# Kernel optimization log

Measured on AMD Instinct MI355X. Metric: run time of the kernel, lower is better.

## Reference

```python
import jax, jax.numpy as jnp
import numpy as np

B, Q, H, V = 32, 180, 768, 19004


def setup_inputs() -> dict:
    key = jax.random.key(0)
    k1, k2, k3, k4 = jax.random.split(key, 4)
    output_tokens = jax.random.normal(k1, (B, Q, H), dtype=jnp.float32)
    W_embed = jax.random.normal(k2, (V, H), dtype=jnp.float32) * 0.02
    b_embed = jax.random.normal(k3, (V,), dtype=jnp.float32) * 0.02
    parcel_ids = jax.random.randint(k4, (V,), 0, Q, dtype=jnp.int32)
    return {"output_tokens": output_tokens, "W_embed": W_embed,
            "b_embed": b_embed, "parcel_ids": parcel_ids}


def reference(output_tokens, W_embed, b_embed, parcel_ids):
    # embed: Linear(hidden_dim -> num_hemi_voxels): [B, Q, V]
    pred = jnp.einsum('bqh,vh->bqv', output_tokens, W_embed) + b_embed
    # movedim(1, -1): [B, V, Q]
    pred = jnp.moveaxis(pred, 1, -1)
    # parcel_mask: one-hot [V, Q] (each voxel assigned to exactly one parcel)
    num_q = output_tokens.shape[1]
    mask = jax.nn.one_hot(parcel_ids, num_q, dtype=pred.dtype)  # [V, Q]
    # multiply by mask and sum over parcel/query axis -> [B, V]
    return jnp.sum(pred * mask, axis=-1)
```

## Files before the change

### kernel.cpp

```cpp
#include <hip/hip_runtime.h>
#include <hip/hip_bf16.h>

#define BB 32
#define QQ 180
#define HH 768
#define VV 19004
#define VB 64
#define KH 384
#define SB 19008
#define MAXDESC 480
#define STRIDE 392

#define WS_NTOT   2048
#define WS_SORTED 4096
#define WS_POSOF  81920
#define WS_DESC   159744
#define WS_RES    167936

typedef __attribute__((ext_vector_type(8))) short short8v;
typedef __attribute__((ext_vector_type(4))) float f32x4;

__device__ __forceinline__ short f2bf(float f) {
    unsigned u = __builtin_bit_cast(unsigned, f);
    u += 0x7FFFu + ((u >> 16) & 1u);
    return (short)(u >> 16);
}

__global__ void prep_k(const int* __restrict__ pid, int* __restrict__ sorted,
                       int* __restrict__ posOf, int4* __restrict__ desc,
                       int* __restrict__ ntot) {
    __shared__ int cnt[256];
    __shared__ int sc[256];
    __shared__ int sn[256];
    __shared__ int cur[256];
    const int t = threadIdx.x;
    if (t < 256) cnt[t] = 0;
    __syncthreads();
    for (int v = t; v < VV; v += 1024) atomicAdd(&cnt[pid[v]], 1);
    __syncthreads();
    if (t < 256) sc[t] = cnt[t];
    __syncthreads();
    for (int off = 1; off < 256; off <<= 1) {
        int add = (t < 256 && t >= off) ? sc[t - off] : 0;
        __syncthreads();
        if (t < 256) sc[t] += add;
        __syncthreads();
    }
    if (t < 256) {
        const int c = cnt[t];
        cur[t] = sc[t] - c;
        sn[t] = (c + VB - 1) / VB;
    }
    __syncthreads();
    for (int off = 1; off < 256; off <<= 1) {
        int add = (t < 256 && t >= off) ? sn[t - off] : 0;
        __syncthreads();
        if (t < 256) sn[t] += add;
        __syncthreads();
    }
    if (t < QQ) {
        const int c = cnt[t];
        const int nch = (c + VB - 1) / VB;
        const int cb = sn[t] - nch;
        const int qs = cur[t];
        for (int j = 0; j < nch; ++j)
            desc[cb + j] = make_int4(t, qs + j * VB, min(VB, c - j * VB), 0);
    }
    if (t == 255) *ntot = sn[255];
    __syncthreads();
    for (int v = t; v < VV; v += 1024) {
        const int q = pid[v];
        const int pos = atomicAdd(&cur[q], 1);
        sorted[pos] = v;
        posOf[v] = pos;
    }
}

__launch_bounds__(256)
__global__ void main_k(const float* __restrict__ OT, const float* __restrict__ W,
                       const int* __restrict__ sorted, const int4* __restrict__ desc,
                       const int* __restrict__ ntot, float* __restrict__ res) {
    const int nt = *ntot;
    const int bid = blockIdx.x;
    const int ci = bid >> 1;
    if (ci >= nt) return;
    const int kh = bid & 1;
    const int4 d = desc[ci];
    const int q     = __builtin_amdgcn_readfirstlane(d.x);
    const int start = __builtin_amdgcn_readfirstlane(d.y);
    const int len   = __builtin_amdgcn_readfirstlane(d.z);
    const int tid = threadIdx.x;

    __shared__ short OTlds[BB * STRIDE];

    {
        const int r = tid >> 3;
        const int o = tid & 7;
        const float* src = OT + ((size_t)r * QQ + q) * HH + kh * KH + o * 8;
        short* dst = &OTlds[r * STRIDE + o * 8];
#pragma unroll
        for (int it = 0; it < 6; ++it) {
            const float4 f0 = *(const float4*)(src + it * 64);
            const float4 f1 = *(const float4*)(src + it * 64 + 4);
            short8v s;
            s[0] = f2bf(f0.x); s[1] = f2bf(f0.y); s[2] = f2bf(f0.z); s[3] = f2bf(f0.w);
            s[4] = f2bf(f1.x); s[5] = f2bf(f1.y); s[6] = f2bf(f1.z); s[7] = f2bf(f1.w);
            *(short8v*)(dst + it * 64) = s;
        }
    }

    const int lane = tid & 63;
    const int w = tid >> 6;
    const int co = lane & 15;
    const int kq = lane >> 4;
    const int vl = 16 * w + co;
    const int vg = sorted[start + min(vl, len - 1)];
    const float4* wp4 = (const float4*)(W + (size_t)vg * HH + kh * KH + kq * 8);
    const short* a0 = &OTlds[co * STRIDE + kq * 8];

    float4 wf[24];
#pragma unroll
    for (int kk = 0; kk < 12; ++kk) {
        wf[2 * kk]     = wp4[kk * 8];
        wf[2 * kk + 1] = wp4[kk * 8 + 1];
    }

    __syncthreads();

    f32x4 acc0 = {0.f, 0.f, 0.f, 0.f};
    f32x4 acc1 = {0.f, 0.f, 0.f, 0.f};
#pragma unroll
    for (int kk = 0; kk < 12; ++kk) {
        const float4 wf0 = wf[2 * kk];
        const float4 wf1 = wf[2 * kk + 1];
        short8v bf;
        bf[0] = f2bf(wf0.x); bf[1] = f2bf(wf0.y); bf[2] = f2bf(wf0.z); bf[3] = f2bf(wf0.w);
        bf[4] = f2bf(wf1.x); bf[5] = f2bf(wf1.y); bf[6] = f2bf(wf1.z); bf[7] = f2bf(wf1.w);
        const short8v a0v = *(const short8v*)(a0 + kk * 32);
        const short8v a1v = *(const short8v*)(a0 + 16 * STRIDE + kk * 32);
        acc0 = __builtin_amdgcn_mfma_f32_16x16x32_bf16(a0v, bf, acc0, 0, 0, 0);
        acc1 = __builtin_amdgcn_mfma_f32_16x16x32_bf16(a1v, bf, acc1, 0, 0, 0);
    }

    if (vl < len) {
        float* rp = res + (size_t)(kh * BB) * SB + start + vl;
#pragma unroll
        for (int r2 = 0; r2 < 4; ++r2) {
            rp[(size_t)(kq * 4 + r2) * SB]      = acc0[r2];
            rp[(size_t)(16 + kq * 4 + r2) * SB] = acc1[r2];
        }
    }
}

__global__ void combine_k(const float* __restrict__ res, const int* __restrict__ posOf,
                          const float* __restrict__ bias, float* __restrict__ out) {
    const int v = blockIdx.x * 256 + threadIdx.x;
    if (v >= VV) return;
    const int b = blockIdx.y;
    const int pos = posOf[v];
    const float s = res[(size_t)b * SB + pos] + res[(size_t)(BB + b) * SB + pos];
    out[(size_t)b * VV + v] = s + bias[v];
}

extern "C" void kernel_launch(void* const* d_in, const int* in_sizes, int n_in,
                              void* d_out, int out_size, void* d_ws, size_t ws_size,
                              hipStream_t stream) {
    const float* OT   = (const float*)d_in[0];
    const float* W    = (const float*)d_in[1];
    const float* bias = (const float*)d_in[2];
    const int*   pid  = (const int*)d_in[3];
    float* out = (float*)d_out;

    char* ws = (char*)d_ws;
    int*   ntot   = (int*)(ws + WS_NTOT);
    int*   sorted = (int*)(ws + WS_SORTED);
    int*   posOf  = (int*)(ws + WS_POSOF);
    int4*  desc   = (int4*)(ws + WS_DESC);
    float* res    = (float*)(ws + WS_RES);

    prep_k<<<1, 1024, 0, stream>>>(pid, sorted, posOf, desc, ntot);

    main_k<<<2 * MAXDESC, 256, 0, stream>>>(OT, W, sorted, desc, ntot, res);

    combine_k<<<dim3((VV + 255) / 256, BB), 256, 0, stream>>>(res, posOf, bias, out);
}
```

Baseline: 49.87 us.

## Split hidden dim into four K-slices, use packed bf16 convert, privatize prep histograms

Splits the H reduction across four blocks per chunk instead of two, halving each block's register load buffer and LDS tile and doubling grid parallelism. Adds a four-way partial-sum combine. Replaces manual bf16 rounding with the hardware v_cvt_pk_bf16_f32 instruction. Prep kernel uses four privatized histograms and counters to cut LDS atomic contention. The costs are more partial-result traffic in the workspace, more redundant sorted/desc loads, and an extra read per output in combine.

```diff
diff --git a/kernel.cpp b/kernel.cpp
--- a/kernel.cpp
+++ b/kernel.cpp
@@ -6,10 +6,10 @@
 #define HH 768
 #define VV 19004
 #define VB 64
-#define KH 384
+#define KQ 192
 #define SB 19008
 #define MAXDESC 480
-#define STRIDE 392
+#define ST 200
 
 #define WS_NTOT   2048
 #define WS_SORTED 4096
@@ -20,57 +20,59 @@
 typedef __attribute__((ext_vector_type(8))) short short8v;
 typedef __attribute__((ext_vector_type(4))) float f32x4;
 
-__device__ __forceinline__ short f2bf(float f) {
-    unsigned u = __builtin_bit_cast(unsigned, f);
-    u += 0x7FFFu + ((u >> 16) & 1u);
-    return (short)(u >> 16);
+__device__ __forceinline__ int cvt_pk_bf16(float lo, float hi) {
+    int r;
+    asm("v_cvt_pk_bf16_f32 %0, %1, %2" : "=v"(r) : "v"(lo), "v"(hi));
+    return r;
 }
 
 __global__ void prep_k(const int* __restrict__ pid, int* __restrict__ sorted,
                        int* __restrict__ posOf, int4* __restrict__ desc,
                        int* __restrict__ ntot) {
-    __shared__ int cnt[256];
+    __shared__ int cnt4[4][256];
+    __shared__ int cur4[4][256];
     __shared__ int sc[256];
     __shared__ int sn[256];
-    __shared__ int cur[256];
     const int t = threadIdx.x;
-    if (t < 256) cnt[t] = 0;
+    const int g = t & 3;
+    ((int*)cnt4)[t] = 0;
     __syncthreads();
-    for (int v = t; v < VV; v += 1024) atomicAdd(&cnt[pid[v]], 1);
+    for (int v = t; v < VV; v += 1024) atomicAdd(&cnt4[g][pid[v]], 1);
     __syncthreads();
-    if (t < 256) sc[t] = cnt[t];
-    __syncthreads();
-    for (int off = 1; off < 256; off <<= 1) {
-        int add = (t < 256 && t >= off) ? sc[t - off] : 0;
-        __syncthreads();
-        if (t < 256) sc[t] += add;
-        __syncthreads();
-    }
+    int c0 = 0, c1 = 0, c2 = 0, c = 0;
     if (t < 256) {
-        const int c = cnt[t];
-        cur[t] = sc[t] - c;
+        c0 = cnt4[0][t]; c1 = cnt4[1][t]; c2 = cnt4[2][t];
+        c = c0 + c1 + c2 + cnt4[3][t];
+        sc[t] = c;
         sn[t] = (c + VB - 1) / VB;
     }
     __syncthreads();
     for (int off = 1; off < 256; off <<= 1) {
-        int add = (t < 256 && t >= off) ? sn[t - off] : 0;
+        int a1 = (t < 256 && t >= off) ? sc[t - off] : 0;
+        int a2 = (t < 256 && t >= off) ? sn[t - off] : 0;
         __syncthreads();
-        if (t < 256) sn[t] += add;
+        if (t < 256) { sc[t] += a1; sn[t] += a2; }
         __syncthreads();
     }
+    if (t < 256) {
+        const int base = sc[t] - c;
+        cur4[0][t] = base;
+        cur4[1][t] = base + c0;
+        cur4[2][t] = base + c0 + c1;
+        cur4[3][t] = base + c0 + c1 + c2;
+    }
     if (t < QQ) {
-        const int c = cnt[t];
         const int nch = (c + VB - 1) / VB;
         const int cb = sn[t] - nch;
-        const int qs = cur[t];
+        const int base = sc[t] - c;
         for (int j = 0; j < nch; ++j)
-            desc[cb + j] = make_int4(t, qs + j * VB, min(VB, c - j * VB), 0);
+            desc[cb + j] = make_int4(t, base + j * VB, min(VB, c - j * VB), 0);
     }
     if (t == 255) *ntot = sn[255];
     __syncthreads();
     for (int v = t; v < VV; v += 1024) {
         const int q = pid[v];
-        const int pos = atomicAdd(&cur[q], 1);
+        const int pos = atomicAdd(&cur4[g][q], 1);
         sorted[pos] = v;
         posOf[v] = pos;
     }
@@ -82,30 +84,31 @@
                        const int* __restrict__ ntot, float* __restrict__ res) {
     const int nt = *ntot;
     const int bid = blockIdx.x;
-    const int ci = bid >> 1;
+    const int ci = bid >> 2;
     if (ci >= nt) return;
-    const int kh = bid & 1;
+    const int kh = bid & 3;
     const int4 d = desc[ci];
     const int q     = __builtin_amdgcn_readfirstlane(d.x);
     const int start = __builtin_amdgcn_readfirstlane(d.y);
     const int len   = __builtin_amdgcn_readfirstlane(d.z);
     const int tid = threadIdx.x;
 
-    __shared__ short OTlds[BB * STRIDE];
+    __shared__ short OTlds[BB * ST];
 
     {
         const int r = tid >> 3;
         const int o = tid & 7;
-        const float* src = OT + ((size_t)r * QQ + q) * HH + kh * KH + o * 8;
-        short* dst = &OTlds[r * STRIDE + o * 8];
+        const float* src = OT + ((size_t)r * QQ + q) * HH + kh * KQ + o * 8;
 #pragma unroll
-        for (int it = 0; it < 6; ++it) {
+        for (int it = 0; it < 3; ++it) {
             const float4 f0 = *(const float4*)(src + it * 64);
             const float4 f1 = *(const float4*)(src + it * 64 + 4);
-            short8v s;
-            s[0] = f2bf(f0.x); s[1] = f2bf(f0.y); s[2] = f2bf(f0.z); s[3] = f2bf(f0.w);
-            s[4] = f2bf(f1.x); s[5] = f2bf(f1.y); s[6] = f2bf(f1.z); s[7] = f2bf(f1.w);
-            *(short8v*)(dst + it * 64) = s;
+            int4 p;
+            p.x = cvt_pk_bf16(f0.x, f0.y);
+            p.y = cvt_pk_bf16(f0.z, f0.w);
+            p.z = cvt_pk_bf16(f1.x, f1.y);
+            p.w = cvt_pk_bf16(f1.z, f1.w);
+            *(int4*)&OTlds[r * ST + it * 64 + o * 8] = p;
         }
     }
 
@@ -115,29 +118,33 @@
     const int kq = lane >> 4;
     const int vl = 16 * w + co;
     const int vg = sorted[start + min(vl, len - 1)];
-    const float4* wp4 = (const float4*)(W + (size_t)vg * HH + kh * KH + kq * 8);
-    const short* a0 = &OTlds[co * STRIDE + kq * 8];
+    const float4* wp4 = (const float4*)(W + (size_t)vg * HH + kh * KQ + kq * 8);
 
-    float4 wf[24];
+    float4 wf[12];
 #pragma unroll
-    for (int kk = 0; kk < 12; ++kk) {
+    for (int kk = 0; kk < 6; ++kk) {
         wf[2 * kk]     = wp4[kk * 8];
         wf[2 * kk + 1] = wp4[kk * 8 + 1];
     }
+
+    const short* a0 = &OTlds[co * ST + kq * 8];
 
     __syncthreads();
 
     f32x4 acc0 = {0.f, 0.f, 0.f, 0.f};
     f32x4 acc1 = {0.f, 0.f, 0.f, 0.f};
 #pragma unroll
-    for (int kk = 0; kk < 12; ++kk) {
+    for (int kk = 0; kk < 6; ++kk) {
         const float4 wf0 = wf[2 * kk];
         const float4 wf1 = wf[2 * kk + 1];
-        short8v bf;
-        bf[0] = f2bf(wf0.x); bf[1] = f2bf(wf0.y); bf[2] = f2bf(wf0.z); bf[3] = f2bf(wf0.w);
-        bf[4] = f2bf(wf1.x); bf[5] = f2bf(wf1.y); bf[6] = f2bf(wf1.z); bf[7] = f2bf(wf1.w);
+        int4 p;
+        p.x = cvt_pk_bf16(wf0.x, wf0.y);
+        p.y = cvt_pk_bf16(wf0.z, wf0.w);
+        p.z = cvt_pk_bf16(wf1.x, wf1.y);
+        p.w = cvt_pk_bf16(wf1.z, wf1.w);
+        const short8v bf = __builtin_bit_cast(short8v, p);
         const short8v a0v = *(const short8v*)(a0 + kk * 32);
-        const short8v a1v = *(const short8v*)(a0 + 16 * STRIDE + kk * 32);
+        const short8v a1v = *(const short8v*)(a0 + 16 * ST + kk * 32);
         acc0 = __builtin_amdgcn_mfma_f32_16x16x32_bf16(a0v, bf, acc0, 0, 0, 0);
         acc1 = __builtin_amdgcn_mfma_f32_16x16x32_bf16(a1v, bf, acc1, 0, 0, 0);
     }
@@ -158,7 +165,10 @@
     if (v >= VV) return;
     const int b = blockIdx.y;
     const int pos = posOf[v];
-    const float s = res[(size_t)b * SB + pos] + res[(size_t)(BB + b) * SB + pos];
+    const float s = res[(size_t)b * SB + pos]
+                  + res[(size_t)(BB + b) * SB + pos]
+                  + res[(size_t)(2 * BB + b) * SB + pos]
+                  + res[(size_t)(3 * BB + b) * SB + pos];
     out[(size_t)b * VV + v] = s + bias[v];
 }
 
@@ -180,7 +190,7 @@
 
     prep_k<<<1, 1024, 0, stream>>>(pid, sorted, posOf, desc, ntot);
 
-    main_k<<<2 * MAXDESC, 256, 0, stream>>>(OT, W, sorted, desc, ntot, res);
+    main_k<<<4 * MAXDESC, 256, 0, stream>>>(OT, W, sorted, desc, ntot, res);
 
     combine_k<<<dim3((VV + 255) / 256, BB), 256, 0, stream>>>(res, posOf, bias, out);
 }
```

Measured after the change: 62.14 us. 24.6% more time.

## Parallelize counting sort prep across blocks with histogram, scan, scatter kernels

Applied to the files above, without the earlier changes.

Replaces the single-block prep kernel with three kernels: per-block histograms over 80 chunks of voxels, a single-block scan that builds chunk descriptors and per-block base offsets, and a multi-block scatter. The aim is to cut the serial latency of one 1024-thread block walking all 19004 voxels with shared atomics. In exchange it adds two extra kernel launches and a serial 80-step loop per parcel inside the scan kernel.

```diff
diff --git a/kernel.cpp b/kernel.cpp
--- a/kernel.cpp
+++ b/kernel.cpp
@@ -10,12 +10,16 @@
 #define SB 19008
 #define MAXDESC 480
 #define STRIDE 392
-
-#define WS_NTOT   2048
-#define WS_SORTED 4096
-#define WS_POSOF  81920
-#define WS_DESC   159744
-#define WS_RES    167936
+#define NB 80
+#define CH 238
+
+#define WS_H      0
+#define WS_BASE   65536
+#define WS_NTOT   131072
+#define WS_DESC   132096
+#define WS_SORTED 140288
+#define WS_POSOF  217088
+#define WS_RES    294912
 
 typedef __attribute__((ext_vector_type(8))) short short8v;
 typedef __attribute__((ext_vector_type(4))) float f32x4;
@@ -26,49 +30,64 @@
     return (short)(u >> 16);
 }
 
-__global__ void prep_k(const int* __restrict__ pid, int* __restrict__ sorted,
-                       int* __restrict__ posOf, int4* __restrict__ desc,
-                       int* __restrict__ ntot) {
-    __shared__ int cnt[256];
-    __shared__ int sc[256];
-    __shared__ int sn[256];
-    __shared__ int cur[256];
+__global__ void hist_k(const int* __restrict__ pid, int* __restrict__ h) {
+    __shared__ int lc[QQ];
+    const int t = threadIdx.x, b = blockIdx.x;
+    if (t < QQ) lc[t] = 0;
+    __syncthreads();
+    const int v = b * CH + t;
+    if (t < CH && v < VV) atomicAdd(&lc[pid[v]], 1);
+    __syncthreads();
+    if (t < QQ) h[b * QQ + t] = lc[t];
+}
+
+__global__ void scan_k(const int* __restrict__ h, int* __restrict__ base,
+                       int4* __restrict__ desc, int* __restrict__ ntot) {
+    __shared__ int s1[256];
+    __shared__ int s2[256];
     const int t = threadIdx.x;
-    if (t < 256) cnt[t] = 0;
-    __syncthreads();
-    for (int v = t; v < VV; v += 1024) atomicAdd(&cnt[pid[v]], 1);
-    __syncthreads();
-    if (t < 256) sc[t] = cnt[t];
+    int c = 0;
+    if (t < QQ)
+        for (int i = 0; i < NB; ++i) c += h[i * QQ + t];
+    s1[t] = c;
     __syncthreads();
     for (int off = 1; off < 256; off <<= 1) {
-        int add = (t < 256 && t >= off) ? sc[t - off] : 0;
-        __syncthreads();
-        if (t < 256) sc[t] += add;
-        __syncthreads();
-    }
-    if (t < 256) {
-        const int c = cnt[t];
-        cur[t] = sc[t] - c;
-        sn[t] = (c + VB - 1) / VB;
-    }
+        int a = (t >= off) ? s1[t - off] : 0;
+        __syncthreads();
+        s1[t] += a;
+        __syncthreads();
+    }
+    const int qs = s1[t] - c;
+    const int nch = (c + VB - 1) / VB;
+    s2[t] = nch;
     __syncthreads();
     for (int off = 1; off < 256; off <<= 1) {
-        int add = (t < 256 && t >= off) ? sn[t - off] : 0;
-        __syncthreads();
-        if (t < 256) sn[t] += add;
+        int a = (t >= off) ? s2[t - off] : 0;
+        __syncthreads();
+        s2[t] += a;
         __syncthreads();
     }
     if (t < QQ) {
-        const int c = cnt[t];
-        const int nch = (c + VB - 1) / VB;
-        const int cb = sn[t] - nch;
-        const int qs = cur[t];
+        const int cb = s2[t] - nch;
         for (int j = 0; j < nch; ++j)
             desc[cb + j] = make_int4(t, qs + j * VB, min(VB, c - j * VB), 0);
-    }
-    if (t == 255) *ntot = sn[255];
-    __syncthreads();
-    for (int v = t; v < VV; v += 1024) {
+        int run = qs;
+        for (int i = 0; i < NB; ++i) {
+            base[i * QQ + t] = run;
+            run += h[i * QQ + t];
+        }
+    }
+    if (t == 255) *ntot = s2[255];
+}
+
+__global__ void scatter_k(const int* __restrict__ pid, const int* __restrict__ base,
+                          int* __restrict__ sorted, int* __restrict__ posOf) {
+    __shared__ int cur[QQ];
+    const int t = threadIdx.x, b = blockIdx.x;
+    if (t < QQ) cur[t] = base[b * QQ + t];
+    __syncthreads();
+    const int v = b * CH + t;
+    if (t < CH && v < VV) {
         const int q = pid[v];
         const int pos = atomicAdd(&cur[q], 1);
         sorted[pos] = v;
@@ -172,13 +191,17 @@
     float* out = (float*)d_out;
 
     char* ws = (char*)d_ws;
+    int*   h      = (int*)(ws + WS_H);
+    int*   base   = (int*)(ws + WS_BASE);
     int*   ntot   = (int*)(ws + WS_NTOT);
+    int4*  desc   = (int4*)(ws + WS_DESC);
     int*   sorted = (int*)(ws + WS_SORTED);
     int*   posOf  = (int*)(ws + WS_POSOF);
-    int4*  desc   = (int4*)(ws + WS_DESC);
     float* res    = (float*)(ws + WS_RES);
 
-    prep_k<<<1, 1024, 0, stream>>>(pid, sorted, posOf, desc, ntot);
+    hist_k<<<NB, 256, 0, stream>>>(pid, h);
+    scan_k<<<1, 256, 0, stream>>>(h, base, desc, ntot);
+    scatter_k<<<NB, 256, 0, stream>>>(pid, base, sorted, posOf);
 
     main_k<<<2 * MAXDESC, 256, 0, stream>>>(OT, W, sorted, desc, ntot, res);
 
```

New measurement: 45.07 us. 1.11x faster.
